# Performance work log

Hardware: AMD Instinct MI355X
Metric: run time of the kernel (lower is better)

Reference implementation:

```python
import jax, jax.numpy as jnp
import numpy as np

B, L, D = 8, 2048, 128
CLIP_MEAN = 1.0
CLIP_STD = 10.0
U = 2.0
SMALL_LOG_STD = -10.0


def setup_inputs() -> dict:
    key = jax.random.key(0)
    ks = jax.random.split(key, 11)
    s = 1.0 / np.sqrt(D).astype(np.float32)
    inp = {
        "query": jax.random.normal(ks[0], (B, L, D), jnp.float32),
        "key": jax.random.normal(ks[1], (B, L, D), jnp.float32),
        "mask": jax.random.randint(ks[2], (B, L, L), 0, 2, jnp.int32),
        "Wq_mean": jax.random.normal(ks[3], (D, D), jnp.float32) * s,
        "bq_mean": jax.random.normal(ks[4], (D,), jnp.float32) * 0.01,
        "Wk_mean": jax.random.normal(ks[5], (D, D), jnp.float32) * s,
        "bk_mean": jax.random.normal(ks[6], (D,), jnp.float32) * 0.01,
        "Wq_std": jax.random.normal(ks[7], (D, D), jnp.float32) * s,
        "bq_std": jax.random.normal(ks[8], (D,), jnp.float32) * 0.01,
        "Wk_std": jax.random.normal(ks[9], (D, D), jnp.float32) * s,
        "bk_std": jax.random.normal(ks[10], (D,), jnp.float32) * 0.01,
    }
    return inp


def _scores(q, k):
    d_k = k.shape[-1]
    return jnp.einsum("bqd,bkd->bqk", q, k) / jnp.sqrt(jnp.asarray(d_k, q.dtype))


def reference(query, key, mask, Wq_mean, bq_mean, Wk_mean, bk_mean, Wq_std, bq_std, Wk_std, bk_std):
    # Linear projections (torch Linear: y = x @ W^T + b; here W stored as [in, out])
    qm = query @ Wq_mean + bq_mean
    km = key @ Wk_mean + bk_mean
    qs = query @ Wq_std + bq_std
    ks = key @ Wk_std + bk_std

    m = mask != 0  # [B, Lq, Lk]

    s_mean = _scores(qm, km)
    s_mean = CLIP_MEAN * (jnp.tanh(s_mean) + 1.0) * 0.5
    s_mean = jnp.where(m, s_mean, 0.0)

    s_std = _scores(qs, ks)
    s_std = (CLIP_STD - U) * ((jnp.tanh(s_std) - 1.0) * 0.5) - U
    s_std = jnp.where(m, s_std, SMALL_LOG_STD)

    return (s_mean, s_std)
```

## Files before the change

kernel.cpp:

```cpp
#include <hip/hip_runtime.h>


#define B_ 8
#define L_ 2048
#define D_ 128
#define NP (B_ * L_ * D_)
#define BLL ((size_t)B_ * L_ * L_)

typedef __attribute__((ext_vector_type(8))) short short8;
typedef __attribute__((ext_vector_type(4))) float f32x4;

__device__ __forceinline__ unsigned short f32_bf16(float x) {
  unsigned u = __float_as_uint(x);
  u += 0x7FFF + ((u >> 16) & 1);
  return (unsigned short)(u >> 16);
}
__device__ __forceinline__ float bf16_f32(unsigned short h) {
  return __uint_as_float(((unsigned)h) << 16);
}
__device__ __forceinline__ float fast_tanh(float x) {
  float e = __expf(2.0f * x);
  return 1.0f - 2.0f * __builtin_amdgcn_rcpf(e + 1.0f);
}

__global__ __launch_bounds__(256) void prep_w(
    const float* __restrict__ w0, const float* __restrict__ w1,
    const float* __restrict__ w2, const float* __restrict__ w3,
    unsigned short* __restrict__ WT) {
  int p = blockIdx.x;
  const float* W = (p == 0) ? w0 : (p == 1) ? w1 : (p == 2) ? w2 : w3;
  int idx = blockIdx.y * 256 + threadIdx.x;
  int k = idx >> 7, n = idx & 127;
  float v = W[idx];
  unsigned short h = f32_bf16(v);
  WT[p * 16384 + n * 128 + k] = h;
  WT[(4 + p) * 16384 + n * 128 + k] = f32_bf16(v - bf16_f32(h));
}

__global__ __launch_bounds__(256) void proj_k(
    const float* __restrict__ query, const float* __restrict__ key,
    const float* __restrict__ bqm, const float* __restrict__ bkm,
    const float* __restrict__ bqs, const float* __restrict__ bks,
    const unsigned short* __restrict__ WT,
    unsigned short* __restrict__ P) {
  const int y = blockIdx.y;
  const float* x = y ? key : query;
  const float* bias_m = y ? bkm : bqm;
  const float* bias_s = y ? bks : bqs;
  const int pm = y, ps = y + 2;
  const int wave = threadIdx.x >> 6, lane = threadIdx.x & 63;
  const int lr = lane & 15, kq = lane >> 4;
  const int rowbase = blockIdx.x * 64 + wave * 16;

  const unsigned short* wmh = WT + pm * 16384;
  const unsigned short* wml = WT + (4 + pm) * 16384;
  const unsigned short* wsh = WT + ps * 16384;
  const unsigned short* wsl = WT + (4 + ps) * 16384;

  f32x4 accm[8], accs[8];
#pragma unroll
  for (int i = 0; i < 8; i++) {
    accm[i] = f32x4{0.f, 0.f, 0.f, 0.f};
    accs[i] = f32x4{0.f, 0.f, 0.f, 0.f};
  }

#pragma unroll
  for (int ks = 0; ks < 4; ks++) {
    const int koff = ks * 32 + kq * 8;
    const float* xp = x + (size_t)(rowbase + lr) * D_ + koff;
    short8 a_hi, a_lo;
#pragma unroll
    for (int j = 0; j < 8; j++) {
      float v = xp[j];
      unsigned short h = f32_bf16(v);
      a_hi[j] = (short)h;
      a_lo[j] = (short)f32_bf16(v - bf16_f32(h));
    }
#pragma unroll
    for (int nt = 0; nt < 8; nt++) {
      const int wo = (nt * 16 + lr) * 128 + koff;
      short8 bh = *(const short8*)(wmh + wo);
      short8 bl = *(const short8*)(wml + wo);
      accm[nt] = __builtin_amdgcn_mfma_f32_16x16x32_bf16(a_hi, bh, accm[nt], 0, 0, 0);
      accm[nt] = __builtin_amdgcn_mfma_f32_16x16x32_bf16(a_lo, bh, accm[nt], 0, 0, 0);
      accm[nt] = __builtin_amdgcn_mfma_f32_16x16x32_bf16(a_hi, bl, accm[nt], 0, 0, 0);
      short8 ch = *(const short8*)(wsh + wo);
      short8 cl = *(const short8*)(wsl + wo);
      accs[nt] = __builtin_amdgcn_mfma_f32_16x16x32_bf16(a_hi, ch, accs[nt], 0, 0, 0);
      accs[nt] = __builtin_amdgcn_mfma_f32_16x16x32_bf16(a_lo, ch, accs[nt], 0, 0, 0);
      accs[nt] = __builtin_amdgcn_mfma_f32_16x16x32_bf16(a_hi, cl, accs[nt], 0, 0, 0);
    }
  }

  unsigned short* Pmh = P + pm * NP;
  unsigned short* Pml = P + (4 + pm) * NP;
  unsigned short* Psh = P + ps * NP;
  unsigned short* Psl = P + (4 + ps) * NP;
#pragma unroll
  for (int nt = 0; nt < 8; nt++) {
    const int col = nt * 16 + lr;
    const float bm = bias_m[col];
    const float bs = bias_s[col];
#pragma unroll
    for (int r = 0; r < 4; r++) {
      const int token = rowbase + kq * 4 + r;
      const int o = token * D_ + col;
      float vm = accm[nt][r] + bm;
      unsigned short h = f32_bf16(vm);
      Pmh[o] = h;
      Pml[o] = f32_bf16(vm - bf16_f32(h));
      float vs = accs[nt][r] + bs;
      unsigned short g = f32_bf16(vs);
      Psh[o] = g;
      Psl[o] = f32_bf16(vs - bf16_f32(g));
    }
  }
}

__global__ __launch_bounds__(256, 2) void scores_k(
    const unsigned short* __restrict__ P,
    const int* __restrict__ mask,
    float* __restrict__ out) {
  const int b = blockIdx.z;
  const int q0 = blockIdx.y * 128, c0 = blockIdx.x * 128;
  const int wave = threadIdx.x >> 6, lane = threadIdx.x & 63;
  const int wr = wave >> 1, wc = wave & 1;
  const int lr = lane & 15, kq = lane >> 4;

  const int qrow = b * L_ + q0 + wr * 64;
  const int crow = b * L_ + c0 + wc * 64;
  const unsigned short* Qmh = P + 0 * NP + (size_t)qrow * D_;
  const unsigned short* Qml = P + 4 * NP + (size_t)qrow * D_;
  const unsigned short* Kmh = P + 1 * NP + (size_t)crow * D_;
  const unsigned short* Kml = P + 5 * NP + (size_t)crow * D_;
  const unsigned short* Qsh = P + 2 * NP + (size_t)qrow * D_;
  const unsigned short* Qsl = P + 6 * NP + (size_t)qrow * D_;
  const unsigned short* Ksh = P + 3 * NP + (size_t)crow * D_;
  const unsigned short* Ksl = P + 7 * NP + (size_t)crow * D_;

  f32x4 am[4][4], as_[4][4];
#pragma unroll
  for (int i = 0; i < 4; i++)
#pragma unroll
    for (int j = 0; j < 4; j++) {
      am[i][j] = f32x4{0.f, 0.f, 0.f, 0.f};
      as_[i][j] = f32x4{0.f, 0.f, 0.f, 0.f};
    }

#pragma unroll
  for (int ks = 0; ks < 4; ks++) {
    const int koff = ks * 32 + kq * 8;
    short8 qh[4], ql[4], kh[4], kl[4];
#pragma unroll
    for (int t = 0; t < 4; t++) {
      const int ro = (t * 16 + lr) * D_ + koff;
      qh[t] = *(const short8*)(Qmh + ro);
      ql[t] = *(const short8*)(Qml + ro);
      kh[t] = *(const short8*)(Kmh + ro);
      kl[t] = *(const short8*)(Kml + ro);
    }
#pragma unroll
    for (int mi = 0; mi < 4; mi++)
#pragma unroll
      for (int ni = 0; ni < 4; ni++) {
        am[mi][ni] = __builtin_amdgcn_mfma_f32_16x16x32_bf16(qh[mi], kh[ni], am[mi][ni], 0, 0, 0);
        am[mi][ni] = __builtin_amdgcn_mfma_f32_16x16x32_bf16(ql[mi], kh[ni], am[mi][ni], 0, 0, 0);
        am[mi][ni] = __builtin_amdgcn_mfma_f32_16x16x32_bf16(qh[mi], kl[ni], am[mi][ni], 0, 0, 0);
      }
#pragma unroll
    for (int t = 0; t < 4; t++) {
      const int ro = (t * 16 + lr) * D_ + koff;
      qh[t] = *(const short8*)(Qsh + ro);
      ql[t] = *(const short8*)(Qsl + ro);
      kh[t] = *(const short8*)(Ksh + ro);
      kl[t] = *(const short8*)(Ksl + ro);
    }
#pragma unroll
    for (int mi = 0; mi < 4; mi++)
#pragma unroll
      for (int ni = 0; ni < 4; ni++) {
        as_[mi][ni] = __builtin_amdgcn_mfma_f32_16x16x32_bf16(qh[mi], kh[ni], as_[mi][ni], 0, 0, 0);
        as_[mi][ni] = __builtin_amdgcn_mfma_f32_16x16x32_bf16(ql[mi], kh[ni], as_[mi][ni], 0, 0, 0);
        as_[mi][ni] = __builtin_amdgcn_mfma_f32_16x16x32_bf16(qh[mi], kl[ni], as_[mi][ni], 0, 0, 0);
      }
  }

  const float rs = 0.08838834764831845f;
#pragma unroll
  for (int mi = 0; mi < 4; mi++) {
#pragma unroll
    for (int r = 0; r < 4; r++) {
      const int q = q0 + wr * 64 + mi * 16 + kq * 4 + r;
      const size_t ob = ((size_t)b * L_ + q) * L_;
      const int kb = c0 + wc * 64;
#pragma unroll
      for (int ni = 0; ni < 4; ni++) {
        const int k = kb + ni * 16 + lr;
        const int mv = mask[ob + k];
        float tm = fast_tanh(am[mi][ni][r] * rs);
        out[ob + k] = mv ? (0.5f * tm + 0.5f) : 0.0f;
        float ts = fast_tanh(as_[mi][ni][r] * rs);
        out[BLL + ob + k] = mv ? (4.0f * ts - 6.0f) : -10.0f;
      }
    }
  }
}

extern "C" void kernel_launch(void* const* d_in, const int* in_sizes, int n_in,
                              void* d_out, int out_size, void* d_ws, size_t ws_size,
                              hipStream_t stream) {
  const float* query = (const float*)d_in[0];
  const float* key   = (const float*)d_in[1];
  const int*   mask  = (const int*)d_in[2];
  const float* Wqm   = (const float*)d_in[3];
  const float* bqm   = (const float*)d_in[4];
  const float* Wkm   = (const float*)d_in[5];
  const float* bkm   = (const float*)d_in[6];
  const float* Wqs   = (const float*)d_in[7];
  const float* bqs   = (const float*)d_in[8];
  const float* Wks   = (const float*)d_in[9];
  const float* bks   = (const float*)d_in[10];

  unsigned short* P  = (unsigned short*)d_ws;
  unsigned short* WT = P + 8 * NP;

  prep_w<<<dim3(4, 64), 256, 0, stream>>>(Wqm, Wkm, Wqs, Wks, WT);
  proj_k<<<dim3(256, 2), 256, 0, stream>>>(query, key, bqm, bkm, bqs, bks, WT, P);
  scores_k<<<dim3(16, 16, 8), 256, 0, stream>>>(P, mask, (float*)d_out);
}
```

Measured before the change: 663.5 us.

## Stage score tiles through LDS for coalesced vector mask/output access; pre-split inputs

The scores epilogue now writes each accumulator tile into a swizzled 64KB shared-memory buffer, then reads it back row-major so mask loads and output stores become 16-byte coalesced vector accesses. The mask bits are cached in a register bitmask so the second (std) output pass does not reload the mask. A separate split_x kernel pre-converts query/key into bf16 hi/lo planes so the projection kernel loads vectors instead of doing scalar float loads and conversion. The 64KB LDS per block may limit occupancy, and there is an extra kernel launch and workspace round-trip.

```diff
diff --git a/kernel.cpp b/kernel.cpp
--- a/kernel.cpp
+++ b/kernel.cpp
@@ -37,14 +37,45 @@
   WT[(4 + p) * 16384 + n * 128 + k] = f32_bf16(v - bf16_f32(h));
 }
 
+__global__ __launch_bounds__(256) void split_x(
+    const float* __restrict__ q, const float* __restrict__ k,
+    unsigned short* __restrict__ XS) {
+  size_t idx = ((size_t)blockIdx.x * 256 + threadIdx.x) * 8;
+  const float* src;
+  unsigned short* dh;
+  if (idx < (size_t)NP) {
+    src = q + idx;
+    dh = XS + idx;
+  } else {
+    src = k + (idx - NP);
+    dh = XS + 2 * (size_t)NP + (idx - NP);
+  }
+  unsigned short* dl = dh + NP;
+  f32x4 v0 = *(const f32x4*)src;
+  f32x4 v1 = *(const f32x4*)(src + 4);
+  short8 h, l;
+#pragma unroll
+  for (int j = 0; j < 4; j++) {
+    unsigned short hh = f32_bf16(v0[j]);
+    h[j] = (short)hh;
+    l[j] = (short)f32_bf16(v0[j] - bf16_f32(hh));
+    unsigned short hg = f32_bf16(v1[j]);
+    h[4 + j] = (short)hg;
+    l[4 + j] = (short)f32_bf16(v1[j] - bf16_f32(hg));
+  }
+  *(short8*)dh = h;
+  *(short8*)dl = l;
+}
+
 __global__ __launch_bounds__(256) void proj_k(
-    const float* __restrict__ query, const float* __restrict__ key,
+    const unsigned short* __restrict__ XS,
     const float* __restrict__ bqm, const float* __restrict__ bkm,
     const float* __restrict__ bqs, const float* __restrict__ bks,
     const unsigned short* __restrict__ WT,
     unsigned short* __restrict__ P) {
   const int y = blockIdx.y;
-  const float* x = y ? key : query;
+  const unsigned short* Xh = XS + (size_t)y * 2 * NP;
+  const unsigned short* Xl = Xh + NP;
   const float* bias_m = y ? bkm : bqm;
   const float* bias_s = y ? bks : bqs;
   const int pm = y, ps = y + 2;
@@ -67,15 +98,9 @@
 #pragma unroll
   for (int ks = 0; ks < 4; ks++) {
     const int koff = ks * 32 + kq * 8;
-    const float* xp = x + (size_t)(rowbase + lr) * D_ + koff;
-    short8 a_hi, a_lo;
-#pragma unroll
-    for (int j = 0; j < 8; j++) {
-      float v = xp[j];
-      unsigned short h = f32_bf16(v);
-      a_hi[j] = (short)h;
-      a_lo[j] = (short)f32_bf16(v - bf16_f32(h));
-    }
+    const int ao = (rowbase + lr) * D_ + koff;
+    short8 a_hi = *(const short8*)(Xh + ao);
+    short8 a_lo = *(const short8*)(Xl + ao);
 #pragma unroll
     for (int nt = 0; nt < 8; nt++) {
       const int wo = (nt * 16 + lr) * 128 + koff;
@@ -123,20 +148,23 @@
     float* __restrict__ out) {
   const int b = blockIdx.z;
   const int q0 = blockIdx.y * 128, c0 = blockIdx.x * 128;
-  const int wave = threadIdx.x >> 6, lane = threadIdx.x & 63;
+  const int tid = threadIdx.x;
+  const int wave = tid >> 6, lane = tid & 63;
   const int wr = wave >> 1, wc = wave & 1;
   const int lr = lane & 15, kq = lane >> 4;
 
+  __shared__ float lt[128 * 128];
+
   const int qrow = b * L_ + q0 + wr * 64;
   const int crow = b * L_ + c0 + wc * 64;
-  const unsigned short* Qmh = P + 0 * NP + (size_t)qrow * D_;
-  const unsigned short* Qml = P + 4 * NP + (size_t)qrow * D_;
-  const unsigned short* Kmh = P + 1 * NP + (size_t)crow * D_;
-  const unsigned short* Kml = P + 5 * NP + (size_t)crow * D_;
-  const unsigned short* Qsh = P + 2 * NP + (size_t)qrow * D_;
-  const unsigned short* Qsl = P + 6 * NP + (size_t)qrow * D_;
-  const unsigned short* Ksh = P + 3 * NP + (size_t)crow * D_;
-  const unsigned short* Ksl = P + 7 * NP + (size_t)crow * D_;
+  const unsigned short* Qmh = P + 0 * (size_t)NP + (size_t)qrow * D_;
+  const unsigned short* Qml = P + 4 * (size_t)NP + (size_t)qrow * D_;
+  const unsigned short* Kmh = P + 1 * (size_t)NP + (size_t)crow * D_;
+  const unsigned short* Kml = P + 5 * (size_t)NP + (size_t)crow * D_;
+  const unsigned short* Qsh = P + 2 * (size_t)NP + (size_t)qrow * D_;
+  const unsigned short* Qsl = P + 6 * (size_t)NP + (size_t)qrow * D_;
+  const unsigned short* Ksh = P + 3 * (size_t)NP + (size_t)crow * D_;
+  const unsigned short* Ksl = P + 7 * (size_t)NP + (size_t)crow * D_;
 
   f32x4 am[4][4], as_[4][4];
 #pragma unroll
@@ -186,23 +214,73 @@
   }
 
   const float rs = 0.08838834764831845f;
-#pragma unroll
-  for (int mi = 0; mi < 4; mi++) {
+
+#pragma unroll
+  for (int mi = 0; mi < 4; mi++)
 #pragma unroll
     for (int r = 0; r < 4; r++) {
-      const int q = q0 + wr * 64 + mi * 16 + kq * 4 + r;
-      const size_t ob = ((size_t)b * L_ + q) * L_;
-      const int kb = c0 + wc * 64;
+      const int row = wr * 64 + mi * 16 + kq * 4 + r;
+      const int xr = ((row >> 2) & 3) << 4;
 #pragma unroll
       for (int ni = 0; ni < 4; ni++) {
-        const int k = kb + ni * 16 + lr;
-        const int mv = mask[ob + k];
-        float tm = fast_tanh(am[mi][ni][r] * rs);
-        out[ob + k] = mv ? (0.5f * tm + 0.5f) : 0.0f;
-        float ts = fast_tanh(as_[mi][ni][r] * rs);
-        out[BLL + ob + k] = mv ? (4.0f * ts - 6.0f) : -10.0f;
+        const int col = wc * 64 + ni * 16 + lr;
+        lt[row * 128 + (col ^ xr)] = am[mi][ni][r];
       }
     }
+  __syncthreads();
+
+  unsigned long long mbits = 0ull;
+#pragma unroll
+  for (int it = 0; it < 16; it++) {
+    const int idx = it * 256 + tid;
+    const int row = idx >> 5;
+    const int c4 = (idx & 31) * 4;
+    const int xr = ((row >> 2) & 3) << 4;
+    f32x4 v = *(const f32x4*)&lt[row * 128 + (c4 ^ xr)];
+    const size_t ob = ((size_t)(b * L_ + q0 + row)) * L_ + c0 + c4;
+    int4 m4 = *(const int4*)&mask[ob];
+    int mv[4] = {m4.x, m4.y, m4.z, m4.w};
+    f32x4 o;
+#pragma unroll
+    for (int j = 0; j < 4; j++) {
+      float tm = fast_tanh(v[j] * rs);
+      o[j] = mv[j] ? (0.5f * tm + 0.5f) : 0.0f;
+      if (mv[j]) mbits |= (1ull << (it * 4 + j));
+    }
+    *(f32x4*)&out[ob] = o;
+  }
+  __syncthreads();
+
+#pragma unroll
+  for (int mi = 0; mi < 4; mi++)
+#pragma unroll
+    for (int r = 0; r < 4; r++) {
+      const int row = wr * 64 + mi * 16 + kq * 4 + r;
+      const int xr = ((row >> 2) & 3) << 4;
+#pragma unroll
+      for (int ni = 0; ni < 4; ni++) {
+        const int col = wc * 64 + ni * 16 + lr;
+        lt[row * 128 + (col ^ xr)] = as_[mi][ni][r];
+      }
+    }
+  __syncthreads();
+
+#pragma unroll
+  for (int it = 0; it < 16; it++) {
+    const int idx = it * 256 + tid;
+    const int row = idx >> 5;
+    const int c4 = (idx & 31) * 4;
+    const int xr = ((row >> 2) & 3) << 4;
+    f32x4 v = *(const f32x4*)&lt[row * 128 + (c4 ^ xr)];
+    const size_t ob = ((size_t)(b * L_ + q0 + row)) * L_ + c0 + c4;
+    f32x4 o;
+#pragma unroll
+    for (int j = 0; j < 4; j++) {
+      float ts = fast_tanh(v[j] * rs);
+      const bool mv = (mbits >> (it * 4 + j)) & 1ull;
+      o[j] = mv ? (4.0f * ts - 6.0f) : -10.0f;
+    }
+    *(f32x4*)&out[BLL + ob] = o;
   }
 }
 
@@ -222,9 +300,11 @@
   const float* bks   = (const float*)d_in[10];
 
   unsigned short* P  = (unsigned short*)d_ws;
-  unsigned short* WT = P + 8 * NP;
+  unsigned short* WT = P + 8 * (size_t)NP;
+  unsigned short* XS = WT + 8 * 16384;
 
   prep_w<<<dim3(4, 64), 256, 0, stream>>>(Wqm, Wkm, Wqs, Wks, WT);
-  proj_k<<<dim3(256, 2), 256, 0, stream>>>(query, key, bqm, bkm, bqs, bks, WT, P);
+  split_x<<<dim3(2048), 256, 0, stream>>>(query, key, XS);
+  proj_k<<<dim3(256, 2), 256, 0, stream>>>(XS, bqm, bkm, bqs, bks, WT, P);
   scores_k<<<dim3(16, 16, 8), 256, 0, stream>>>(P, mask, (float*)d_out);
 }
```

After: 596.5 us. 1.11x faster.

## Restructure scores kernel with 32x32 MFMA, sequential passes, mask bitcache, presplit inputs

Applied to the files above, without the earlier changes.

The scores kernel now computes the mean and std products one after the other with 32x32x16 MFMA tiles instead of 16x16x32, which cuts accumulator registers so launch bounds can rise to four blocks per SM. The mask is read only in the first pass and kept as a 64-bit per-thread bitmask for the second pass. Blocks are linearised with batch as the fastest index. A new split_x kernel precomputes the bf16 hi/lo split of query/key so proj_k loads it directly, at the cost of an extra launch and extra workspace traffic. The output stores keep a 32-column-contiguous pattern per row.

```diff
diff --git a/kernel.cpp b/kernel.cpp
--- a/kernel.cpp
+++ b/kernel.cpp
@@ -9,6 +9,7 @@
 
 typedef __attribute__((ext_vector_type(8))) short short8;
 typedef __attribute__((ext_vector_type(4))) float f32x4;
+typedef __attribute__((ext_vector_type(16))) float f32x16;
 
 __device__ __forceinline__ unsigned short f32_bf16(float x) {
   unsigned u = __float_as_uint(x);
@@ -37,14 +38,45 @@
   WT[(4 + p) * 16384 + n * 128 + k] = f32_bf16(v - bf16_f32(h));
 }
 
+__global__ __launch_bounds__(256) void split_x(
+    const float* __restrict__ q, const float* __restrict__ k,
+    unsigned short* __restrict__ XS) {
+  size_t idx = ((size_t)blockIdx.x * 256 + threadIdx.x) * 8;
+  const float* src;
+  unsigned short* dh;
+  if (idx < (size_t)NP) {
+    src = q + idx;
+    dh = XS + idx;
+  } else {
+    src = k + (idx - NP);
+    dh = XS + 2 * (size_t)NP + (idx - NP);
+  }
+  unsigned short* dl = dh + NP;
+  f32x4 v0 = *(const f32x4*)src;
+  f32x4 v1 = *(const f32x4*)(src + 4);
+  short8 h, l;
+#pragma unroll
+  for (int j = 0; j < 4; j++) {
+    unsigned short hh = f32_bf16(v0[j]);
+    h[j] = (short)hh;
+    l[j] = (short)f32_bf16(v0[j] - bf16_f32(hh));
+    unsigned short hg = f32_bf16(v1[j]);
+    h[4 + j] = (short)hg;
+    l[4 + j] = (short)f32_bf16(v1[j] - bf16_f32(hg));
+  }
+  *(short8*)dh = h;
+  *(short8*)dl = l;
+}
+
 __global__ __launch_bounds__(256) void proj_k(
-    const float* __restrict__ query, const float* __restrict__ key,
+    const unsigned short* __restrict__ XS,
     const float* __restrict__ bqm, const float* __restrict__ bkm,
     const float* __restrict__ bqs, const float* __restrict__ bks,
     const unsigned short* __restrict__ WT,
     unsigned short* __restrict__ P) {
   const int y = blockIdx.y;
-  const float* x = y ? key : query;
+  const unsigned short* Xh = XS + (size_t)y * 2 * NP;
+  const unsigned short* Xl = Xh + NP;
   const float* bias_m = y ? bkm : bqm;
   const float* bias_s = y ? bks : bqs;
   const int pm = y, ps = y + 2;
@@ -67,15 +99,9 @@
 #pragma unroll
   for (int ks = 0; ks < 4; ks++) {
     const int koff = ks * 32 + kq * 8;
-    const float* xp = x + (size_t)(rowbase + lr) * D_ + koff;
-    short8 a_hi, a_lo;
-#pragma unroll
-    for (int j = 0; j < 8; j++) {
-      float v = xp[j];
-      unsigned short h = f32_bf16(v);
-      a_hi[j] = (short)h;
-      a_lo[j] = (short)f32_bf16(v - bf16_f32(h));
-    }
+    const int ao = (rowbase + lr) * D_ + koff;
+    short8 a_hi = *(const short8*)(Xh + ao);
+    short8 a_lo = *(const short8*)(Xl + ao);
 #pragma unroll
     for (int nt = 0; nt < 8; nt++) {
       const int wo = (nt * 16 + lr) * 128 + koff;
@@ -117,90 +143,82 @@
   }
 }
 
-__global__ __launch_bounds__(256, 2) void scores_k(
+__global__ __launch_bounds__(256, 4) void scores_k(
     const unsigned short* __restrict__ P,
     const int* __restrict__ mask,
     float* __restrict__ out) {
-  const int b = blockIdx.z;
-  const int q0 = blockIdx.y * 128, c0 = blockIdx.x * 128;
+  const int bid = blockIdx.x;
+  const int z = bid & 7;
+  const int idx = bid >> 3;
+  const int q0 = (idx >> 4) * 128, c0 = (idx & 15) * 128;
   const int wave = threadIdx.x >> 6, lane = threadIdx.x & 63;
   const int wr = wave >> 1, wc = wave & 1;
-  const int lr = lane & 15, kq = lane >> 4;
-
-  const int qrow = b * L_ + q0 + wr * 64;
-  const int crow = b * L_ + c0 + wc * 64;
-  const unsigned short* Qmh = P + 0 * NP + (size_t)qrow * D_;
-  const unsigned short* Qml = P + 4 * NP + (size_t)qrow * D_;
-  const unsigned short* Kmh = P + 1 * NP + (size_t)crow * D_;
-  const unsigned short* Kml = P + 5 * NP + (size_t)crow * D_;
-  const unsigned short* Qsh = P + 2 * NP + (size_t)qrow * D_;
-  const unsigned short* Qsl = P + 6 * NP + (size_t)qrow * D_;
-  const unsigned short* Ksh = P + 3 * NP + (size_t)crow * D_;
-  const unsigned short* Ksl = P + 7 * NP + (size_t)crow * D_;
-
-  f32x4 am[4][4], as_[4][4];
-#pragma unroll
-  for (int i = 0; i < 4; i++)
-#pragma unroll
-    for (int j = 0; j < 4; j++) {
-      am[i][j] = f32x4{0.f, 0.f, 0.f, 0.f};
-      as_[i][j] = f32x4{0.f, 0.f, 0.f, 0.f};
-    }
-
-#pragma unroll
-  for (int ks = 0; ks < 4; ks++) {
-    const int koff = ks * 32 + kq * 8;
-    short8 qh[4], ql[4], kh[4], kl[4];
-#pragma unroll
-    for (int t = 0; t < 4; t++) {
-      const int ro = (t * 16 + lr) * D_ + koff;
-      qh[t] = *(const short8*)(Qmh + ro);
-      ql[t] = *(const short8*)(Qml + ro);
-      kh[t] = *(const short8*)(Kmh + ro);
-      kl[t] = *(const short8*)(Kml + ro);
-    }
-#pragma unroll
-    for (int mi = 0; mi < 4; mi++)
-#pragma unroll
-      for (int ni = 0; ni < 4; ni++) {
-        am[mi][ni] = __builtin_amdgcn_mfma_f32_16x16x32_bf16(qh[mi], kh[ni], am[mi][ni], 0, 0, 0);
-        am[mi][ni] = __builtin_amdgcn_mfma_f32_16x16x32_bf16(ql[mi], kh[ni], am[mi][ni], 0, 0, 0);
-        am[mi][ni] = __builtin_amdgcn_mfma_f32_16x16x32_bf16(qh[mi], kl[ni], am[mi][ni], 0, 0, 0);
+  const int lc = lane & 31, lh = lane >> 5;
+
+  const float rs = 0.08838834764831845f;
+  unsigned long long mbits = 0ull;
+
+  for (int p = 0; p < 2; ++p) {
+    const unsigned short* Qh = P + (size_t)(2 * p) * NP;
+    const unsigned short* Ql = Qh + 4 * (size_t)NP;
+    const unsigned short* Kh = P + (size_t)(2 * p + 1) * NP;
+    const unsigned short* Kl = Kh + 4 * (size_t)NP;
+
+    const int qr0 = (z * L_ + q0 + wr * 64) * D_;
+    const int cr0 = (z * L_ + c0 + wc * 64) * D_;
+
+    f32x16 acc[2][2];
+#pragma unroll
+    for (int i = 0; i < 2; i++)
+#pragma unroll
+      for (int j = 0; j < 2; j++)
+#pragma unroll
+        for (int r = 0; r < 16; r++) acc[i][j][r] = 0.0f;
+
+#pragma unroll
+    for (int kk = 0; kk < 8; ++kk) {
+      const int ko = kk * 16 + lh * 8;
+      short8 ah[2], al[2], bh[2], bl[2];
+#pragma unroll
+      for (int t = 0; t < 2; t++) {
+        const int aoff = qr0 + (t * 32 + lc) * D_ + ko;
+        ah[t] = *(const short8*)(Qh + aoff);
+        al[t] = *(const short8*)(Ql + aoff);
+        const int boff = cr0 + (t * 32 + lc) * D_ + ko;
+        bh[t] = *(const short8*)(Kh + boff);
+        bl[t] = *(const short8*)(Kl + boff);
       }
 #pragma unroll
-    for (int t = 0; t < 4; t++) {
-      const int ro = (t * 16 + lr) * D_ + koff;
-      qh[t] = *(const short8*)(Qsh + ro);
-      ql[t] = *(const short8*)(Qsl + ro);
-      kh[t] = *(const short8*)(Ksh + ro);
-      kl[t] = *(const short8*)(Ksl + ro);
-    }
-#pragma unroll
-    for (int mi = 0; mi < 4; mi++)
-#pragma unroll
-      for (int ni = 0; ni < 4; ni++) {
-        as_[mi][ni] = __builtin_amdgcn_mfma_f32_16x16x32_bf16(qh[mi], kh[ni], as_[mi][ni], 0, 0, 0);
-        as_[mi][ni] = __builtin_amdgcn_mfma_f32_16x16x32_bf16(ql[mi], kh[ni], as_[mi][ni], 0, 0, 0);
-        as_[mi][ni] = __builtin_amdgcn_mfma_f32_16x16x32_bf16(qh[mi], kl[ni], as_[mi][ni], 0, 0, 0);
-      }
-  }
-
-  const float rs = 0.08838834764831845f;
-#pragma unroll
-  for (int mi = 0; mi < 4; mi++) {
-#pragma unroll
-    for (int r = 0; r < 4; r++) {
-      const int q = q0 + wr * 64 + mi * 16 + kq * 4 + r;
-      const size_t ob = ((size_t)b * L_ + q) * L_;
-      const int kb = c0 + wc * 64;
-#pragma unroll
-      for (int ni = 0; ni < 4; ni++) {
-        const int k = kb + ni * 16 + lr;
-        const int mv = mask[ob + k];
-        float tm = fast_tanh(am[mi][ni][r] * rs);
-        out[ob + k] = mv ? (0.5f * tm + 0.5f) : 0.0f;
-        float ts = fast_tanh(as_[mi][ni][r] * rs);
-        out[BLL + ob + k] = mv ? (4.0f * ts - 6.0f) : -10.0f;
+      for (int tr = 0; tr < 2; tr++)
+#pragma unroll
+        for (int tc = 0; tc < 2; tc++) {
+          acc[tr][tc] = __builtin_amdgcn_mfma_f32_32x32x16_bf16(ah[tr], bh[tc], acc[tr][tc], 0, 0, 0);
+          acc[tr][tc] = __builtin_amdgcn_mfma_f32_32x32x16_bf16(al[tr], bh[tc], acc[tr][tc], 0, 0, 0);
+          acc[tr][tc] = __builtin_amdgcn_mfma_f32_32x32x16_bf16(ah[tr], bl[tc], acc[tr][tc], 0, 0, 0);
+        }
+    }
+
+#pragma unroll
+    for (int tr = 0; tr < 2; tr++) {
+      const int growb = q0 + wr * 64 + tr * 32 + 4 * lh;
+#pragma unroll
+      for (int tc = 0; tc < 2; tc++) {
+        const int gcol = c0 + wc * 64 + tc * 32 + lc;
+#pragma unroll
+        for (int r = 0; r < 16; r++) {
+          const int grow = growb + (r & 3) + 8 * (r >> 2);
+          const size_t a = ((size_t)(z * L_ + grow)) * L_ + gcol;
+          const float t = fast_tanh(acc[tr][tc][r] * rs);
+          const int bi = (tr * 2 + tc) * 16 + r;
+          if (p == 0) {
+            const int mv = mask[a];
+            out[a] = mv ? (0.5f * t + 0.5f) : 0.0f;
+            if (mv) mbits |= (1ull << bi);
+          } else {
+            const bool mv = (mbits >> bi) & 1ull;
+            out[BLL + a] = mv ? (4.0f * t - 6.0f) : -10.0f;
+          }
+        }
       }
     }
   }
@@ -222,9 +240,11 @@
   const float* bks   = (const float*)d_in[10];
 
   unsigned short* P  = (unsigned short*)d_ws;
-  unsigned short* WT = P + 8 * NP;
+  unsigned short* WT = P + 8 * (size_t)NP;
+  unsigned short* XS = WT + 8 * 16384;
 
   prep_w<<<dim3(4, 64), 256, 0, stream>>>(Wqm, Wkm, Wqs, Wks, WT);
-  proj_k<<<dim3(256, 2), 256, 0, stream>>>(query, key, bqm, bkm, bqs, bks, WT, P);
-  scores_k<<<dim3(16, 16, 8), 256, 0, stream>>>(P, mask, (float*)d_out);
-}
+  split_x<<<dim3(2048), 256, 0, stream>>>(query, key, XS);
+  proj_k<<<dim3(256, 2), 256, 0, stream>>>(XS, bqm, bkm, bqs, bks, WT, P);
+  scores_k<<<dim3(2048), 256, 0, stream>>>(P, mask, (float*)d_out);
+}
```

Result: slower. 971.3 us (+46.4%).
